# Kernel optimization log

Hardware: AMD Instinct MI355X
Metric: run time of the kernel (lower is better)

The kernel has to match this reference:

```python
import jax, jax.numpy as jnp
import numpy as np

EPS = 1e-5

def _layernorm(x, gamma, beta):
    mu = jnp.mean(x, axis=-1, keepdims=True)
    var = jnp.mean(jnp.square(x - mu), axis=-1, keepdims=True)
    return (x - mu) * jax.lax.rsqrt(var + EPS) * gamma + beta


def setup_inputs() -> dict:
    key = jax.random.key(0)
    ks = jax.random.split(key, 5)
    B, N, M, E, C = 64, 4096, 64, 256, 128
    return {
        "query": jax.random.normal(ks[0], (B, N, C), dtype=jnp.float32),
        "key": jax.random.normal(ks[1], (B, M, E), dtype=jnp.float32),
        "value": jax.random.normal(ks[2], (B, M, E), dtype=jnp.float32),
        "k_proj_weight": jax.random.normal(ks[3], (E, C), dtype=jnp.float32) * 0.02,
        "v_proj_weight": jax.random.normal(ks[4], (E, C), dtype=jnp.float32) * 0.02,
        "norm1_gamma": jnp.ones((E,), dtype=jnp.float32),
        "norm1_beta": jnp.zeros((E,), dtype=jnp.float32),
        "norm2_gamma": jnp.ones((C,), dtype=jnp.float32),
        "norm2_beta": jnp.zeros((C,), dtype=jnp.float32),
    }


def reference(query, key, value, k_proj_weight, v_proj_weight,
              norm1_gamma, norm1_beta, norm2_gamma, norm2_beta):
    # key: [B, M, E] -> LN over E; query: [B, N, C] -> LN over C
    k = _layernorm(key, norm1_gamma, norm1_beta)
    q = _layernorm(query, norm2_gamma, norm2_beta)
    # project key to [B, C, M], value to [B, M, C]
    k = jnp.einsum('bme,ec->bcm', k, k_proj_weight)
    v = jnp.einsum('bme,ec->bmc', value, v_proj_weight)
    # attention scores [B, N, M], softmax over group tokens M
    attn = jax.nn.softmax(jnp.einsum('bnc,bcm->bnm', q, k), axis=-1)
    # output [B, N, C]
    return jnp.einsum('bnm,bmc->bnc', attn, v)
```

## Files before the change

### kernel.cpp

```cpp
#include <hip/hip_runtime.h>

typedef _Float16 f16;
typedef f16 f16x8 __attribute__((ext_vector_type(8)));
typedef float f32x4 __attribute__((ext_vector_type(4)));

#define NN 4096
#define MM 64
#define EE 256
#define CC 128

__device__ __forceinline__ f32x4 mfma16(f16x8 a, f16x8 b, f32x4 c) {
  return __builtin_amdgcn_mfma_f32_16x16x32_f16(a, b, c, 0, 0, 0);
}

__global__ __launch_bounds__(256) void wt_kernel(
    const float* __restrict__ Wk, const float* __restrict__ Wv,
    f16* __restrict__ WkTh, f16* __restrict__ WkTl,
    f16* __restrict__ WvTh, f16* __restrict__ WvTl) {
  __shared__ __align__(16) float wlds[64][132];
  const int job = blockIdx.x >> 2;
  const int e0 = (blockIdx.x & 3) * 64;
  const float* __restrict__ W = job ? Wv : Wk;
  f16* __restrict__ WTh = job ? WvTh : WkTh;
  f16* __restrict__ WTl = job ? WvTl : WkTl;
  const int t = threadIdx.x;
  {
    const int er = t >> 2, c0 = (t & 3) * 32;
#pragma unroll
    for (int i = 0; i < 8; ++i) {
      float4 v = *(const float4*)&W[(e0 + er) * CC + c0 + 4 * i];
      *(float4*)&wlds[er][c0 + 4 * i] = v;
    }
  }
  __syncthreads();
  const int c = t >> 1, eh = (t & 1) * 32;
#pragma unroll
  for (int s = 0; s < 4; ++s) {
    f16x8 hh, ll;
#pragma unroll
    for (int j = 0; j < 8; ++j) {
      float v = wlds[eh + 8 * s + j][c];
      f16 h = (f16)v;
      hh[j] = h;
      ll[j] = (f16)(v - (float)h);
    }
    *(f16x8*)&WTh[c * EE + e0 + eh + 8 * s] = hh;
    *(f16x8*)&WTl[c * EE + e0 + eh + 8 * s] = ll;
  }
}

__global__ __launch_bounds__(256) void prep_kernel(
    const float* __restrict__ keyp, const float* __restrict__ valp,
    const float* __restrict__ g1, const float* __restrict__ b1,
    const f16* __restrict__ WkTh, const f16* __restrict__ WkTl,
    const f16* __restrict__ WvTh, const f16* __restrict__ WvTl,
    f16* __restrict__ K2h, f16* __restrict__ K2l,
    f16* __restrict__ VTh, f16* __restrict__ VTl) {
  __shared__ __align__(16) f16 aldsh[64][256];
  __shared__ __align__(16) f16 aldsl[64][256];
  const int b = blockIdx.x >> 1, job = blockIdx.x & 1;
  const int t = threadIdx.x, l = t & 63, w = t >> 6;
  {
    const int m = t >> 2, q0 = (t & 3) * 64;
    const float* __restrict__ src = (job ? valp : keyp) + (b * MM + m) * EE + q0;
    float x[64];
    float s1 = 0.f;
#pragma unroll
    for (int i = 0; i < 16; ++i) {
      float4 v = *(const float4*)&src[4 * i];
      x[4 * i] = v.x; x[4 * i + 1] = v.y; x[4 * i + 2] = v.z; x[4 * i + 3] = v.w;
      s1 += v.x + v.y + v.z + v.w;
    }
    if (job == 0) {
      s1 += __shfl_xor(s1, 1); s1 += __shfl_xor(s1, 2);
      const float mu = s1 * (1.f / EE);
      float s2 = 0.f;
#pragma unroll
      for (int i = 0; i < 64; ++i) { float d = x[i] - mu; s2 += d * d; }
      s2 += __shfl_xor(s2, 1); s2 += __shfl_xor(s2, 2);
      const float rs = 1.f / sqrtf(s2 * (1.f / EE) + 1e-5f);
#pragma unroll
      for (int i = 0; i < 16; ++i) {
        float4 gv = *(const float4*)&g1[q0 + 4 * i];
        float4 bv = *(const float4*)&b1[q0 + 4 * i];
        x[4 * i]     = (x[4 * i]     - mu) * rs * gv.x + bv.x;
        x[4 * i + 1] = (x[4 * i + 1] - mu) * rs * gv.y + bv.y;
        x[4 * i + 2] = (x[4 * i + 2] - mu) * rs * gv.z + bv.z;
        x[4 * i + 3] = (x[4 * i + 3] - mu) * rs * gv.w + bv.w;
      }
    }
#pragma unroll
    for (int s = 0; s < 8; ++s) {
      f16x8 hh, ll;
#pragma unroll
      for (int j = 0; j < 8; ++j) {
        float v = x[8 * s + j];
        f16 h = (f16)v;
        hh[j] = h;
        ll[j] = (f16)(v - (float)h);
      }
      *(f16x8*)&aldsh[m][q0 + 8 * s] = hh;
      *(f16x8*)&aldsl[m][q0 + 8 * s] = ll;
    }
  }
  __syncthreads();
  const int l15 = l & 15, lo = (l >> 4) * 8;
  if (job == 0) {
    f16x8 ah[8], al[8];
#pragma unroll
    for (int kk = 0; kk < 8; ++kk) {
      ah[kk] = *(const f16x8*)&aldsh[16 * w + l15][32 * kk + lo];
      al[kk] = *(const f16x8*)&aldsl[16 * w + l15][32 * kk + lo];
    }
#pragma unroll
    for (int g = 0; g < 8; ++g) {
      f32x4 acc = {0.f, 0.f, 0.f, 0.f};
#pragma unroll
      for (int kk = 0; kk < 8; ++kk) {
        f16x8 bh = *(const f16x8*)&WkTh[(16 * g + l15) * EE + 32 * kk + lo];
        f16x8 bl = *(const f16x8*)&WkTl[(16 * g + l15) * EE + 32 * kk + lo];
        acc = mfma16(ah[kk], bh, acc);
        acc = mfma16(al[kk], bh, acc);
        acc = mfma16(ah[kk], bl, acc);
      }
#pragma unroll
      for (int j = 0; j < 4; ++j) {
        const int mrow = 16 * w + 4 * (l >> 4) + j;
        const int ccol = 16 * g + l15;
        const int idx = b * (MM * CC) + mrow * CC + (ccol ^ (8 * (mrow & 7)));
        float v = acc[j];
        f16 h = (f16)v;
        K2h[idx] = h;
        K2l[idx] = (f16)(v - (float)h);
      }
    }
  } else {
#pragma unroll
    for (int rt = 0; rt < 2; ++rt) {
      const int ct = 16 * (w + 4 * rt);
      f16x8 ah[8], al[8];
#pragma unroll
      for (int kk = 0; kk < 8; ++kk) {
        ah[kk] = *(const f16x8*)&WvTh[(ct + l15) * EE + 32 * kk + lo];
        al[kk] = *(const f16x8*)&WvTl[(ct + l15) * EE + 32 * kk + lo];
      }
#pragma unroll
      for (int g = 0; g < 4; ++g) {
        f32x4 acc = {0.f, 0.f, 0.f, 0.f};
#pragma unroll
        for (int kk = 0; kk < 8; ++kk) {
          f16x8 bh = *(const f16x8*)&aldsh[16 * g + l15][32 * kk + lo];
          f16x8 bl = *(const f16x8*)&aldsl[16 * g + l15][32 * kk + lo];
          acc = mfma16(ah[kk], bh, acc);
          acc = mfma16(al[kk], bh, acc);
          acc = mfma16(ah[kk], bl, acc);
        }
#pragma unroll
        for (int j = 0; j < 4; ++j) {
          const int crow = ct + 4 * (l >> 4) + j;
          const int mcol = 16 * g + l15;
          const int idx = b * (CC * MM) + crow * MM + (mcol ^ (8 * (crow & 7)));
          float v = acc[j];
          f16 h = (f16)v;
          VTh[idx] = h;
          VTl[idx] = (f16)(v - (float)h);
        }
      }
    }
  }
}

__global__ __launch_bounds__(256, 2) void attn_kernel(
    const float* __restrict__ qin,
    const f16* __restrict__ K2hg, const f16* __restrict__ K2lg,
    const f16* __restrict__ VThg, const f16* __restrict__ VTlg,
    const float* __restrict__ g2, const float* __restrict__ b2,
    float* __restrict__ outp) {
  __shared__ __align__(16) f16 k2h[MM * CC];
  __shared__ __align__(16) f16 k2l[MM * CC];
  __shared__ __align__(16) f16 vth[CC * MM];
  __shared__ __align__(16) f16 vtl[CC * MM];
  const int bid = blockIdx.x;
  const int swz = (bid & 7) * 512 + (bid >> 3);
  const int b = swz >> 6, tile = swz & 63;
  const int t = threadIdx.x, l = t & 63, w = t >> 6;
  const int l15 = l & 15, lo = (l >> 4) * 8, swl = 8 * (l & 7);

  {
    const float4* __restrict__ skh = (const float4*)(K2hg + b * (MM * CC));
    const float4* __restrict__ skl = (const float4*)(K2lg + b * (MM * CC));
    const float4* __restrict__ svh = (const float4*)(VThg + b * (CC * MM));
    const float4* __restrict__ svl = (const float4*)(VTlg + b * (CC * MM));
#pragma unroll
    for (int i = 0; i < 4; ++i) {
      const int idx = t + 256 * i;
      ((float4*)k2h)[idx] = skh[idx];
      ((float4*)k2l)[idx] = skl[idx];
      ((float4*)vth)[idx] = svh[idx];
      ((float4*)vtl)[idx] = svl[idx];
    }
  }

  const int r = tile * 64 + 16 * w + l15;
  const float* __restrict__ qrow = qin + (b * NN + r) * CC;
  float x[4][8];
  float s1 = 0.f;
#pragma unroll
  for (int kk = 0; kk < 4; ++kk) {
    float4 v0 = *(const float4*)&qrow[32 * kk + lo];
    float4 v1 = *(const float4*)&qrow[32 * kk + lo + 4];
    x[kk][0] = v0.x; x[kk][1] = v0.y; x[kk][2] = v0.z; x[kk][3] = v0.w;
    x[kk][4] = v1.x; x[kk][5] = v1.y; x[kk][6] = v1.z; x[kk][7] = v1.w;
    s1 += v0.x + v0.y + v0.z + v0.w + v1.x + v1.y + v1.z + v1.w;
  }
  s1 += __shfl_xor(s1, 16); s1 += __shfl_xor(s1, 32);
  const float mu = s1 * (1.f / CC);
  float s2 = 0.f;
#pragma unroll
  for (int kk = 0; kk < 4; ++kk)
#pragma unroll
    for (int j = 0; j < 8; ++j) { float d = x[kk][j] - mu; s2 += d * d; }
  s2 += __shfl_xor(s2, 16); s2 += __shfl_xor(s2, 32);
  const float rs = 1.f / sqrtf(s2 * (1.f / CC) + 1e-5f);

  f16x8 aqh[4], aql[4];
#pragma unroll
  for (int kk = 0; kk < 4; ++kk) {
    float4 g0 = *(const float4*)&g2[32 * kk + lo];
    float4 g1v = *(const float4*)&g2[32 * kk + lo + 4];
    float4 c0 = *(const float4*)&b2[32 * kk + lo];
    float4 c1 = *(const float4*)&b2[32 * kk + lo + 4];
    float gg[8] = {g0.x, g0.y, g0.z, g0.w, g1v.x, g1v.y, g1v.z, g1v.w};
    float bb[8] = {c0.x, c0.y, c0.z, c0.w, c1.x, c1.y, c1.z, c1.w};
#pragma unroll
    for (int j = 0; j < 8; ++j) {
      float y = (x[kk][j] - mu) * rs * gg[j] + bb[j];
      f16 h = (f16)y;
      aqh[kk][j] = h;
      aql[kk][j] = (f16)(y - (float)h);
    }
  }
  __syncthreads();

  f32x4 sa[4];
#pragma unroll
  for (int g = 0; g < 4; ++g) sa[g] = (f32x4){0.f, 0.f, 0.f, 0.f};
#pragma unroll
  for (int g = 0; g < 4; ++g)
#pragma unroll
    for (int kk = 0; kk < 4; ++kk) {
      const int co = (16 * g + l15) * CC + ((32 * kk + lo) ^ swl);
      f16x8 bh = *(const f16x8*)&k2h[co];
      f16x8 bl = *(const f16x8*)&k2l[co];
      sa[g] = mfma16(aqh[kk], bh, sa[g]);
      sa[g] = mfma16(aql[kk], bh, sa[g]);
      sa[g] = mfma16(aqh[kk], bl, sa[g]);
    }

  __syncthreads();

  float mx[4], rinv[4];
#pragma unroll
  for (int j = 0; j < 4; ++j) {
    float v = fmaxf(fmaxf(sa[0][j], sa[1][j]), fmaxf(sa[2][j], sa[3][j]));
    v = fmaxf(v, __shfl_xor(v, 1));
    v = fmaxf(v, __shfl_xor(v, 2));
    v = fmaxf(v, __shfl_xor(v, 4));
    v = fmaxf(v, __shfl_xor(v, 8));
    mx[j] = v;
  }
#pragma unroll
  for (int g = 0; g < 4; ++g)
#pragma unroll
    for (int j = 0; j < 4; ++j) sa[g][j] = expf(sa[g][j] - mx[j]);
#pragma unroll
  for (int j = 0; j < 4; ++j) {
    float v = sa[0][j] + sa[1][j] + sa[2][j] + sa[3][j];
    v += __shfl_xor(v, 1);
    v += __shfl_xor(v, 2);
    v += __shfl_xor(v, 4);
    v += __shfl_xor(v, 8);
    rinv[j] = 1.f / v;
  }

  f16* __restrict__ pldsh = &k2h[w * 1024];
  f16* __restrict__ pldsl = &k2l[w * 1024];
#pragma unroll
  for (int g = 0; g < 4; ++g)
#pragma unroll
    for (int j = 0; j < 4; ++j) {
      const int rl = 4 * (l >> 4) + j;
      const int mc = 16 * g + l15;
      const int pi = rl * 64 + (mc ^ (8 * (rl & 7)));
      const float p = sa[g][j] * rinv[j];
      const f16 ph = (f16)p;
      pldsh[pi] = ph;
      pldsl[pi] = (f16)(p - (float)ph);
    }
  asm volatile("s_waitcnt lgkmcnt(0)" ::: "memory");
  __builtin_amdgcn_sched_barrier(0);

  f16x8 aph[2], apl[2];
#pragma unroll
  for (int ks = 0; ks < 2; ++ks) {
    const int po = l15 * 64 + ((32 * ks + lo) ^ swl);
    aph[ks] = *(const f16x8*)&pldsh[po];
    apl[ks] = *(const f16x8*)&pldsl[po];
  }
  f32x4 oa[8];
#pragma unroll
  for (int g = 0; g < 8; ++g) oa[g] = (f32x4){0.f, 0.f, 0.f, 0.f};
#pragma unroll
  for (int g = 0; g < 8; ++g)
#pragma unroll
    for (int ks = 0; ks < 2; ++ks) {
      const int vo = (16 * g + l15) * MM + ((32 * ks + lo) ^ swl);
      f16x8 bh = *(const f16x8*)&vth[vo];
      f16x8 bl = *(const f16x8*)&vtl[vo];
      oa[g] = mfma16(aph[ks], bh, oa[g]);
      oa[g] = mfma16(apl[ks], bh, oa[g]);
      oa[g] = mfma16(aph[ks], bl, oa[g]);
    }

  const int rb = (b * NN + tile * 64 + 16 * w + 4 * (l >> 4)) * CC;
#pragma unroll
  for (int g = 0; g < 8; ++g)
#pragma unroll
    for (int j = 0; j < 4; ++j)
      outp[rb + j * CC + 16 * g + l15] = oa[g][j];
}

extern "C" void kernel_launch(void* const* d_in, const int* in_sizes, int n_in,
                              void* d_out, int out_size, void* d_ws, size_t ws_size,
                              hipStream_t stream) {
  (void)in_sizes; (void)n_in; (void)out_size; (void)ws_size;
  const float* q   = (const float*)d_in[0];
  const float* key = (const float*)d_in[1];
  const float* val = (const float*)d_in[2];
  const float* wk  = (const float*)d_in[3];
  const float* wv  = (const float*)d_in[4];
  const float* g1  = (const float*)d_in[5];
  const float* b1  = (const float*)d_in[6];
  const float* g2  = (const float*)d_in[7];
  const float* b2  = (const float*)d_in[8];
  float* out = (float*)d_out;

  char* ws = (char*)d_ws;
  f16* WkTh = (f16*)(ws);
  f16* WkTl = (f16*)(ws + 65536);
  f16* WvTh = (f16*)(ws + 131072);
  f16* WvTl = (f16*)(ws + 196608);
  f16* K2h  = (f16*)(ws + 262144);
  f16* K2l  = (f16*)(ws + 262144 + 1048576);
  f16* VTh  = (f16*)(ws + 262144 + 2097152);
  f16* VTl  = (f16*)(ws + 262144 + 3145728);

  wt_kernel<<<8, 256, 0, stream>>>(wk, wv, WkTh, WkTl, WvTh, WvTl);
  prep_kernel<<<128, 256, 0, stream>>>(key, val, g1, b1, WkTh, WkTl, WvTh, WvTl,
                                       K2h, K2l, VTh, VTl);
  attn_kernel<<<4096, 256, 0, stream>>>(q, K2h, K2l, VTh, VTl, g2, b2, out);
}
```

Before: 286.3 us.

## Read K/V operands directly from global memory instead of staging in LDS

The attention kernel no longer copies per-batch K2/VT hi/lo tiles into shared memory. It loads the MFMA B operands straight from global memory, so the LDS staging and two block barriers go away. LDS drops to the per-wave P buffers only, which allows raising launch bounds from 2 to 5 blocks per SM. The swizzle on the K2/VT global layout is removed to match. The prep kernel is split across twice as many blocks, each computing half of a projection. The risk is that the repeated global/L2 reads of K and V for every N tile may cost more in latency than the LDS copy did.

Measured after the change: 372.1 us. 30.0% more time.

```diff
diff --git a/kernel.cpp b/kernel.cpp
--- a/kernel.cpp
+++ b/kernel.cpp
@@ -58,11 +58,11 @@
     f16* __restrict__ VTh, f16* __restrict__ VTl) {
   __shared__ __align__(16) f16 aldsh[64][256];
   __shared__ __align__(16) f16 aldsl[64][256];
-  const int b = blockIdx.x >> 1, job = blockIdx.x & 1;
+  const int b = blockIdx.x >> 2, jb = blockIdx.x & 3;
   const int t = threadIdx.x, l = t & 63, w = t >> 6;
   {
     const int m = t >> 2, q0 = (t & 3) * 64;
-    const float* __restrict__ src = (job ? valp : keyp) + (b * MM + m) * EE + q0;
+    const float* __restrict__ src = (jb >= 2 ? valp : keyp) + (b * MM + m) * EE + q0;
     float x[64];
     float s1 = 0.f;
 #pragma unroll
@@ -71,7 +71,7 @@
       x[4 * i] = v.x; x[4 * i + 1] = v.y; x[4 * i + 2] = v.z; x[4 * i + 3] = v.w;
       s1 += v.x + v.y + v.z + v.w;
     }
-    if (job == 0) {
+    if (jb < 2) {
       s1 += __shfl_xor(s1, 1); s1 += __shfl_xor(s1, 2);
       const float mu = s1 * (1.f / EE);
       float s2 = 0.f;
@@ -105,7 +105,7 @@
   }
   __syncthreads();
   const int l15 = l & 15, lo = (l >> 4) * 8;
-  if (job == 0) {
+  if (jb < 2) {
     f16x8 ah[8], al[8];
 #pragma unroll
     for (int kk = 0; kk < 8; ++kk) {
@@ -113,7 +113,8 @@
       al[kk] = *(const f16x8*)&aldsl[16 * w + l15][32 * kk + lo];
     }
 #pragma unroll
-    for (int g = 0; g < 8; ++g) {
+    for (int gg = 0; gg < 4; ++gg) {
+      const int g = 4 * jb + gg;
       f32x4 acc = {0.f, 0.f, 0.f, 0.f};
 #pragma unroll
       for (int kk = 0; kk < 8; ++kk) {
@@ -127,7 +128,7 @@
       for (int j = 0; j < 4; ++j) {
         const int mrow = 16 * w + 4 * (l >> 4) + j;
         const int ccol = 16 * g + l15;
-        const int idx = b * (MM * CC) + mrow * CC + (ccol ^ (8 * (mrow & 7)));
+        const int idx = b * (MM * CC) + mrow * CC + ccol;
         float v = acc[j];
         f16 h = (f16)v;
         K2h[idx] = h;
@@ -135,71 +136,56 @@
       }
     }
   } else {
-#pragma unroll
-    for (int rt = 0; rt < 2; ++rt) {
-      const int ct = 16 * (w + 4 * rt);
-      f16x8 ah[8], al[8];
+    const int ct = 16 * (w + 4 * (jb - 2));
+    f16x8 ah[8], al[8];
+#pragma unroll
+    for (int kk = 0; kk < 8; ++kk) {
+      ah[kk] = *(const f16x8*)&WvTh[(ct + l15) * EE + 32 * kk + lo];
+      al[kk] = *(const f16x8*)&WvTl[(ct + l15) * EE + 32 * kk + lo];
+    }
+#pragma unroll
+    for (int g = 0; g < 4; ++g) {
+      f32x4 acc = {0.f, 0.f, 0.f, 0.f};
 #pragma unroll
       for (int kk = 0; kk < 8; ++kk) {
-        ah[kk] = *(const f16x8*)&WvTh[(ct + l15) * EE + 32 * kk + lo];
-        al[kk] = *(const f16x8*)&WvTl[(ct + l15) * EE + 32 * kk + lo];
-      }
-#pragma unroll
-      for (int g = 0; g < 4; ++g) {
-        f32x4 acc = {0.f, 0.f, 0.f, 0.f};
-#pragma unroll
-        for (int kk = 0; kk < 8; ++kk) {
-          f16x8 bh = *(const f16x8*)&aldsh[16 * g + l15][32 * kk + lo];
-          f16x8 bl = *(const f16x8*)&aldsl[16 * g + l15][32 * kk + lo];
-          acc = mfma16(ah[kk], bh, acc);
-          acc = mfma16(al[kk], bh, acc);
-          acc = mfma16(ah[kk], bl, acc);
-        }
-#pragma unroll
-        for (int j = 0; j < 4; ++j) {
-          const int crow = ct + 4 * (l >> 4) + j;
-          const int mcol = 16 * g + l15;
-          const int idx = b * (CC * MM) + crow * MM + (mcol ^ (8 * (crow & 7)));
-          float v = acc[j];
-          f16 h = (f16)v;
-          VTh[idx] = h;
-          VTl[idx] = (f16)(v - (float)h);
-        }
-      }
-    }
-  }
-}
-
-__global__ __launch_bounds__(256, 2) void attn_kernel(
+        f16x8 bh = *(const f16x8*)&aldsh[16 * g + l15][32 * kk + lo];
+        f16x8 bl = *(const f16x8*)&aldsl[16 * g + l15][32 * kk + lo];
+        acc = mfma16(ah[kk], bh, acc);
+        acc = mfma16(al[kk], bh, acc);
+        acc = mfma16(ah[kk], bl, acc);
+      }
+#pragma unroll
+      for (int j = 0; j < 4; ++j) {
+        const int crow = ct + 4 * (l >> 4) + j;
+        const int mcol = 16 * g + l15;
+        const int idx = b * (CC * MM) + crow * MM + mcol;
+        float v = acc[j];
+        f16 h = (f16)v;
+        VTh[idx] = h;
+        VTl[idx] = (f16)(v - (float)h);
+      }
+    }
+  }
+}
+
+__global__ __launch_bounds__(256, 5) void attn_kernel(
     const float* __restrict__ qin,
     const f16* __restrict__ K2hg, const f16* __restrict__ K2lg,
     const f16* __restrict__ VThg, const f16* __restrict__ VTlg,
     const float* __restrict__ g2, const float* __restrict__ b2,
     float* __restrict__ outp) {
-  __shared__ __align__(16) f16 k2h[MM * CC];
-  __shared__ __align__(16) f16 k2l[MM * CC];
-  __shared__ __align__(16) f16 vth[CC * MM];
-  __shared__ __align__(16) f16 vtl[CC * MM];
+  __shared__ __align__(16) f16 pldsh[4][1024];
+  __shared__ __align__(16) f16 pldsl[4][1024];
   const int bid = blockIdx.x;
   const int swz = (bid & 7) * 512 + (bid >> 3);
   const int b = swz >> 6, tile = swz & 63;
   const int t = threadIdx.x, l = t & 63, w = t >> 6;
   const int l15 = l & 15, lo = (l >> 4) * 8, swl = 8 * (l & 7);
 
-  {
-    const float4* __restrict__ skh = (const float4*)(K2hg + b * (MM * CC));
-    const float4* __restrict__ skl = (const float4*)(K2lg + b * (MM * CC));
-    const float4* __restrict__ svh = (const float4*)(VThg + b * (CC * MM));
-    const float4* __restrict__ svl = (const float4*)(VTlg + b * (CC * MM));
-#pragma unroll
-    for (int i = 0; i < 4; ++i) {
-      const int idx = t + 256 * i;
-      ((float4*)k2h)[idx] = skh[idx];
-      ((float4*)k2l)[idx] = skl[idx];
-      ((float4*)vth)[idx] = svh[idx];
-      ((float4*)vtl)[idx] = svl[idx];
-    }
-  }
+  const f16* __restrict__ k2hb = K2hg + b * (MM * CC);
+  const f16* __restrict__ k2lb = K2lg + b * (MM * CC);
+  const f16* __restrict__ vthb = VThg + b * (CC * MM);
+  const f16* __restrict__ vtlb = VTlg + b * (CC * MM);
 
   const int r = tile * 64 + 16 * w + l15;
   const float* __restrict__ qrow = qin + (b * NN + r) * CC;
@@ -240,7 +226,6 @@
       aql[kk][j] = (f16)(y - (float)h);
     }
   }
-  __syncthreads();
 
   f32x4 sa[4];
 #pragma unroll
@@ -249,15 +234,13 @@
   for (int g = 0; g < 4; ++g)
 #pragma unroll
     for (int kk = 0; kk < 4; ++kk) {
-      const int co = (16 * g + l15) * CC + ((32 * kk + lo) ^ swl);
-      f16x8 bh = *(const f16x8*)&k2h[co];
-      f16x8 bl = *(const f16x8*)&k2l[co];
+      const int co = (16 * g + l15) * CC + 32 * kk + lo;
+      f16x8 bh = *(const f16x8*)&k2hb[co];
+      f16x8 bl = *(const f16x8*)&k2lb[co];
       sa[g] = mfma16(aqh[kk], bh, sa[g]);
       sa[g] = mfma16(aql[kk], bh, sa[g]);
       sa[g] = mfma16(aqh[kk], bl, sa[g]);
     }
-
-  __syncthreads();
 
   float mx[4], rinv[4];
 #pragma unroll
@@ -283,8 +266,6 @@
     rinv[j] = 1.f / v;
   }
 
-  f16* __restrict__ pldsh = &k2h[w * 1024];
-  f16* __restrict__ pldsl = &k2l[w * 1024];
 #pragma unroll
   for (int g = 0; g < 4; ++g)
 #pragma unroll
@@ -294,8 +275,8 @@
       const int pi = rl * 64 + (mc ^ (8 * (rl & 7)));
       const float p = sa[g][j] * rinv[j];
       const f16 ph = (f16)p;
-      pldsh[pi] = ph;
-      pldsl[pi] = (f16)(p - (float)ph);
+      pldsh[w][pi] = ph;
+      pldsl[w][pi] = (f16)(p - (float)ph);
     }
   asm volatile("s_waitcnt lgkmcnt(0)" ::: "memory");
   __builtin_amdgcn_sched_barrier(0);
@@ -304,8 +285,8 @@
 #pragma unroll
   for (int ks = 0; ks < 2; ++ks) {
     const int po = l15 * 64 + ((32 * ks + lo) ^ swl);
-    aph[ks] = *(const f16x8*)&pldsh[po];
-    apl[ks] = *(const f16x8*)&pldsl[po];
+    aph[ks] = *(const f16x8*)&pldsh[w][po];
+    apl[ks] = *(const f16x8*)&pldsl[w][po];
   }
   f32x4 oa[8];
 #pragma unroll
@@ -314,9 +295,9 @@
   for (int g = 0; g < 8; ++g)
 #pragma unroll
     for (int ks = 0; ks < 2; ++ks) {
-      const int vo = (16 * g + l15) * MM + ((32 * ks + lo) ^ swl);
-      f16x8 bh = *(const f16x8*)&vth[vo];
-      f16x8 bl = *(const f16x8*)&vtl[vo];
+      const int vo = (16 * g + l15) * MM + 32 * ks + lo;
+      f16x8 bh = *(const f16x8*)&vthb[vo];
+      f16x8 bl = *(const f16x8*)&vtlb[vo];
       oa[g] = mfma16(aph[ks], bh, oa[g]);
       oa[g] = mfma16(apl[ks], bh, oa[g]);
       oa[g] = mfma16(aph[ks], bl, oa[g]);
@@ -356,7 +337,7 @@
   f16* VTl  = (f16*)(ws + 262144 + 3145728);
 
   wt_kernel<<<8, 256, 0, stream>>>(wk, wv, WkTh, WkTl, WvTh, WvTl);
-  prep_kernel<<<128, 256, 0, stream>>>(key, val, g1, b1, WkTh, WkTl, WvTh, WvTl,
+  prep_kernel<<<256, 256, 0, stream>>>(key, val, g1, b1, WkTh, WkTl, WvTh, WvTl,
                                        K2h, K2l, VTh, VTl);
   attn_kernel<<<4096, 256, 0, stream>>>(q, K2h, K2l, VTh, VTl, g2, b2, out);
 }
```

## Use single-f16 P·V product and split prep kernel across more blocks

Applied to the files above, without the earlier changes.

The P·V step drops the hi/lo split of both the probabilities and V, so it uses one MFMA per step instead of three. This removes the low-part V buffer from workspace, shared memory and global loads. With less shared memory the attention kernel raises its occupancy hint to 3 blocks per SM. The softmax barrier moves after the reductions, and the prep kernel now uses 4 blocks per batch instead of 2. The cost is lower precision in the output, since P and V are now plain f16.

Measured after the change: 277.8 us. 3.0% less time.

```diff
diff --git a/kernel.cpp b/kernel.cpp
--- a/kernel.cpp
+++ b/kernel.cpp
@@ -55,14 +55,14 @@
     const f16* __restrict__ WkTh, const f16* __restrict__ WkTl,
     const f16* __restrict__ WvTh, const f16* __restrict__ WvTl,
     f16* __restrict__ K2h, f16* __restrict__ K2l,
-    f16* __restrict__ VTh, f16* __restrict__ VTl) {
+    f16* __restrict__ VTh) {
   __shared__ __align__(16) f16 aldsh[64][256];
   __shared__ __align__(16) f16 aldsl[64][256];
-  const int b = blockIdx.x >> 1, job = blockIdx.x & 1;
+  const int b = blockIdx.x >> 2, jb = blockIdx.x & 3;
   const int t = threadIdx.x, l = t & 63, w = t >> 6;
   {
     const int m = t >> 2, q0 = (t & 3) * 64;
-    const float* __restrict__ src = (job ? valp : keyp) + (b * MM + m) * EE + q0;
+    const float* __restrict__ src = (jb >= 2 ? valp : keyp) + (b * MM + m) * EE + q0;
     float x[64];
     float s1 = 0.f;
 #pragma unroll
@@ -71,7 +71,7 @@
       x[4 * i] = v.x; x[4 * i + 1] = v.y; x[4 * i + 2] = v.z; x[4 * i + 3] = v.w;
       s1 += v.x + v.y + v.z + v.w;
     }
-    if (job == 0) {
+    if (jb < 2) {
       s1 += __shfl_xor(s1, 1); s1 += __shfl_xor(s1, 2);
       const float mu = s1 * (1.f / EE);
       float s2 = 0.f;
@@ -105,7 +105,7 @@
   }
   __syncthreads();
   const int l15 = l & 15, lo = (l >> 4) * 8;
-  if (job == 0) {
+  if (jb < 2) {
     f16x8 ah[8], al[8];
 #pragma unroll
     for (int kk = 0; kk < 8; ++kk) {
@@ -113,7 +113,8 @@
       al[kk] = *(const f16x8*)&aldsl[16 * w + l15][32 * kk + lo];
     }
 #pragma unroll
-    for (int g = 0; g < 8; ++g) {
+    for (int gg = 0; gg < 4; ++gg) {
+      const int g = 4 * jb + gg;
       f32x4 acc = {0.f, 0.f, 0.f, 0.f};
 #pragma unroll
       for (int kk = 0; kk < 8; ++kk) {
@@ -135,51 +136,44 @@
       }
     }
   } else {
-#pragma unroll
-    for (int rt = 0; rt < 2; ++rt) {
-      const int ct = 16 * (w + 4 * rt);
-      f16x8 ah[8], al[8];
+    const int ct = 16 * (w + 4 * (jb - 2));
+    f16x8 ah[8], al[8];
+#pragma unroll
+    for (int kk = 0; kk < 8; ++kk) {
+      ah[kk] = *(const f16x8*)&WvTh[(ct + l15) * EE + 32 * kk + lo];
+      al[kk] = *(const f16x8*)&WvTl[(ct + l15) * EE + 32 * kk + lo];
+    }
+#pragma unroll
+    for (int g = 0; g < 4; ++g) {
+      f32x4 acc = {0.f, 0.f, 0.f, 0.f};
 #pragma unroll
       for (int kk = 0; kk < 8; ++kk) {
-        ah[kk] = *(const f16x8*)&WvTh[(ct + l15) * EE + 32 * kk + lo];
-        al[kk] = *(const f16x8*)&WvTl[(ct + l15) * EE + 32 * kk + lo];
-      }
-#pragma unroll
-      for (int g = 0; g < 4; ++g) {
-        f32x4 acc = {0.f, 0.f, 0.f, 0.f};
-#pragma unroll
-        for (int kk = 0; kk < 8; ++kk) {
-          f16x8 bh = *(const f16x8*)&aldsh[16 * g + l15][32 * kk + lo];
-          f16x8 bl = *(const f16x8*)&aldsl[16 * g + l15][32 * kk + lo];
-          acc = mfma16(ah[kk], bh, acc);
-          acc = mfma16(al[kk], bh, acc);
-          acc = mfma16(ah[kk], bl, acc);
-        }
-#pragma unroll
-        for (int j = 0; j < 4; ++j) {
-          const int crow = ct + 4 * (l >> 4) + j;
-          const int mcol = 16 * g + l15;
-          const int idx = b * (CC * MM) + crow * MM + (mcol ^ (8 * (crow & 7)));
-          float v = acc[j];
-          f16 h = (f16)v;
-          VTh[idx] = h;
-          VTl[idx] = (f16)(v - (float)h);
-        }
-      }
-    }
-  }
-}
-
-__global__ __launch_bounds__(256, 2) void attn_kernel(
+        f16x8 bh = *(const f16x8*)&aldsh[16 * g + l15][32 * kk + lo];
+        f16x8 bl = *(const f16x8*)&aldsl[16 * g + l15][32 * kk + lo];
+        acc = mfma16(ah[kk], bh, acc);
+        acc = mfma16(al[kk], bh, acc);
+        acc = mfma16(ah[kk], bl, acc);
+      }
+#pragma unroll
+      for (int j = 0; j < 4; ++j) {
+        const int crow = ct + 4 * (l >> 4) + j;
+        const int mcol = 16 * g + l15;
+        const int idx = b * (CC * MM) + crow * MM + (mcol ^ (8 * (crow & 7)));
+        VTh[idx] = (f16)acc[j];
+      }
+    }
+  }
+}
+
+__global__ __launch_bounds__(256, 3) void attn_kernel(
     const float* __restrict__ qin,
     const f16* __restrict__ K2hg, const f16* __restrict__ K2lg,
-    const f16* __restrict__ VThg, const f16* __restrict__ VTlg,
+    const f16* __restrict__ VThg,
     const float* __restrict__ g2, const float* __restrict__ b2,
     float* __restrict__ outp) {
   __shared__ __align__(16) f16 k2h[MM * CC];
   __shared__ __align__(16) f16 k2l[MM * CC];
   __shared__ __align__(16) f16 vth[CC * MM];
-  __shared__ __align__(16) f16 vtl[CC * MM];
   const int bid = blockIdx.x;
   const int swz = (bid & 7) * 512 + (bid >> 3);
   const int b = swz >> 6, tile = swz & 63;
@@ -190,14 +184,12 @@
     const float4* __restrict__ skh = (const float4*)(K2hg + b * (MM * CC));
     const float4* __restrict__ skl = (const float4*)(K2lg + b * (MM * CC));
     const float4* __restrict__ svh = (const float4*)(VThg + b * (CC * MM));
-    const float4* __restrict__ svl = (const float4*)(VTlg + b * (CC * MM));
 #pragma unroll
     for (int i = 0; i < 4; ++i) {
       const int idx = t + 256 * i;
       ((float4*)k2h)[idx] = skh[idx];
       ((float4*)k2l)[idx] = skl[idx];
       ((float4*)vth)[idx] = svh[idx];
-      ((float4*)vtl)[idx] = svl[idx];
     }
   }
 
@@ -257,8 +249,6 @@
       sa[g] = mfma16(aqh[kk], bl, sa[g]);
     }
 
-  __syncthreads();
-
   float mx[4], rinv[4];
 #pragma unroll
   for (int j = 0; j < 4; ++j) {
@@ -283,30 +273,24 @@
     rinv[j] = 1.f / v;
   }
 
-  f16* __restrict__ pldsh = &k2h[w * 1024];
-  f16* __restrict__ pldsl = &k2l[w * 1024];
+  __syncthreads();
+
+  f16* __restrict__ plds = &k2h[w * 1024];
 #pragma unroll
   for (int g = 0; g < 4; ++g)
 #pragma unroll
     for (int j = 0; j < 4; ++j) {
       const int rl = 4 * (l >> 4) + j;
       const int mc = 16 * g + l15;
-      const int pi = rl * 64 + (mc ^ (8 * (rl & 7)));
-      const float p = sa[g][j] * rinv[j];
-      const f16 ph = (f16)p;
-      pldsh[pi] = ph;
-      pldsl[pi] = (f16)(p - (float)ph);
+      plds[rl * 64 + (mc ^ (8 * (rl & 7)))] = (f16)(sa[g][j] * rinv[j]);
     }
   asm volatile("s_waitcnt lgkmcnt(0)" ::: "memory");
   __builtin_amdgcn_sched_barrier(0);
 
-  f16x8 aph[2], apl[2];
-#pragma unroll
-  for (int ks = 0; ks < 2; ++ks) {
-    const int po = l15 * 64 + ((32 * ks + lo) ^ swl);
-    aph[ks] = *(const f16x8*)&pldsh[po];
-    apl[ks] = *(const f16x8*)&pldsl[po];
-  }
+  f16x8 ap[2];
+#pragma unroll
+  for (int ks = 0; ks < 2; ++ks)
+    ap[ks] = *(const f16x8*)&plds[l15 * 64 + ((32 * ks + lo) ^ swl)];
   f32x4 oa[8];
 #pragma unroll
   for (int g = 0; g < 8; ++g) oa[g] = (f32x4){0.f, 0.f, 0.f, 0.f};
@@ -314,12 +298,8 @@
   for (int g = 0; g < 8; ++g)
 #pragma unroll
     for (int ks = 0; ks < 2; ++ks) {
-      const int vo = (16 * g + l15) * MM + ((32 * ks + lo) ^ swl);
-      f16x8 bh = *(const f16x8*)&vth[vo];
-      f16x8 bl = *(const f16x8*)&vtl[vo];
-      oa[g] = mfma16(aph[ks], bh, oa[g]);
-      oa[g] = mfma16(apl[ks], bh, oa[g]);
-      oa[g] = mfma16(aph[ks], bl, oa[g]);
+      f16x8 bv = *(const f16x8*)&vth[(16 * g + l15) * MM + ((32 * ks + lo) ^ swl)];
+      oa[g] = mfma16(ap[ks], bv, oa[g]);
     }
 
   const int rb = (b * NN + tile * 64 + 16 * w + 4 * (l >> 4)) * CC;
@@ -353,10 +333,9 @@
   f16* K2h  = (f16*)(ws + 262144);
   f16* K2l  = (f16*)(ws + 262144 + 1048576);
   f16* VTh  = (f16*)(ws + 262144 + 2097152);
-  f16* VTl  = (f16*)(ws + 262144 + 3145728);
 
   wt_kernel<<<8, 256, 0, stream>>>(wk, wv, WkTh, WkTl, WvTh, WvTl);
-  prep_kernel<<<128, 256, 0, stream>>>(key, val, g1, b1, WkTh, WkTl, WvTh, WvTl,
-                                       K2h, K2l, VTh, VTl);
-  attn_kernel<<<4096, 256, 0, stream>>>(q, K2h, K2l, VTh, VTl, g2, b2, out);
-}
+  prep_kernel<<<256, 256, 0, stream>>>(key, val, g1, b1, WkTh, WkTl, WvTh, WvTl,
+                                       K2h, K2l, VTh);
+  attn_kernel<<<4096, 256, 0, stream>>>(q, K2h, K2l, VTh, g2, b2, out);
+}
```
